# Kernel tuning notes

Measured on AMD Instinct MI355X. Metric: run time of the kernel, lower is better.

## Reference

```python
import jax, jax.numpy as jnp
import numpy as np

VOCAB = 50000   # vocab.count
EMBED = 256     # args.embed
B = 16          # batch
C = 64          # uniform context_len per example (stack() requires it)
S = 512         # src_seq == qry_seq == args.max_in_seq
UNK = 1         # vocab.w2i['<UNK>']


def setup_inputs() -> dict:
    key = jax.random.key(0)
    k1, k2, k3, k4 = jax.random.split(key, 4)
    sources = jax.random.randint(k1, (B * C, S), 0, VOCAB)
    # queries: contiguous nonzero prefix of length q_len in [S//2, S], zeros after
    ids = jax.random.randint(k2, (B, S), 1, VOCAB)
    qlens = jax.random.randint(k3, (B,), S // 2, S + 1)
    queries = jnp.where(jnp.arange(S)[None, :] < qlens[:, None], ids, 0)
    emb = jax.random.normal(k4, (VOCAB, EMBED), dtype=jnp.float32)
    return {"sources": sources, "queries": queries, "context_len": C, "emb": emb}


def reference(sources, queries, context_len, emb):
    vocab = emb.shape[0]
    # unk_tensor: clamp out-of-vocab ids to <UNK>
    src_ids = jnp.where(sources >= vocab, UNK, sources)
    q_ids = jnp.where(queries >= vocab, UNK, queries)
    b, s = queries.shape
    # [b, C, S, D] embedded sources; [b, S, D] embedded queries
    es = emb[src_ids].reshape(b, context_len, s, emb.shape[1])
    eq = emb[q_ids]
    # q_len slicing == masking since nonzero query prefix is contiguous
    qmask = (queries > 0).astype(emb.dtype)            # [b, S]
    # score[b,c] = sum_{j < q_len_b} <es[b,c,j], eq[b,j]>
    scores = jnp.einsum('bcsd,bsd->bc', es, eq * qmask[:, :, None])
    sims = jax.nn.softmax(scores, axis=1)              # per-example softmax over context
    top = jnp.argmax(scores, axis=1)                   # argmax of sim == argmax of scores
    src3 = sources.reshape(b, context_len, s)
    out_sources = jnp.take_along_axis(src3, top[:, None, None], axis=1).squeeze(1)
    return out_sources, sims
```

## Files before the change

### kernel.cpp

```cpp
#include <hip/hip_runtime.h>

#define VOCAB 50000
#define EMBED 256
#define NB    16
#define NC    64
#define NS    512
#define UNK   1

#define NPART 8
#define PDIV  ((VOCAB + NPART - 1) / NPART)
#define PJT   8
#define PJLEN 64
#define WLCAP 1024
#define NSLICE (NPART * PJT)
#define BF_TABLE_BYTES ((size_t)VOCAB * EMBED * 2)
#define PARTIAL_ELEMS  (NSLICE * NB * NC)

__device__ __forceinline__ unsigned short f2bf_rne(float f) {
    unsigned int u = __float_as_uint(f);
    u = (u + 0x7fffu + ((u >> 16) & 1u)) >> 16;
    return (unsigned short)u;
}

__global__ __launch_bounds__(256) void convert_kernel(
    const float* __restrict__ emb, unsigned int* __restrict__ bf)
{
    const size_t t = (size_t)blockIdx.x * 256 + threadIdx.x;
    const float4* __restrict__ e4 = (const float4*)emb;
    const float4 a = e4[t * 2];
    const float4 b = e4[t * 2 + 1];
    uint4 r;
    r.x = (unsigned int)f2bf_rne(a.x) | ((unsigned int)f2bf_rne(a.y) << 16);
    r.y = (unsigned int)f2bf_rne(a.z) | ((unsigned int)f2bf_rne(a.w) << 16);
    r.z = (unsigned int)f2bf_rne(b.x) | ((unsigned int)f2bf_rne(b.y) << 16);
    r.w = (unsigned int)f2bf_rne(b.z) | ((unsigned int)f2bf_rne(b.w) << 16);
    ((uint4*)bf)[t] = r;
}

__device__ __forceinline__ float dot_u(unsigned a, unsigned b) {
    const float a0 = __uint_as_float(a << 16);
    const float a1 = __uint_as_float(a & 0xffff0000u);
    const float b0 = __uint_as_float(b << 16);
    const float b1 = __uint_as_float(b & 0xffff0000u);
    return a0 * b0 + a1 * b1;
}

__global__ __launch_bounds__(256) void scores_part_kernel(
    const int* __restrict__ src, const int* __restrict__ q,
    const unsigned int* __restrict__ bf, float* __restrict__ partial)
{
    const int bid = blockIdx.x;
    const int p   = bid & (NPART - 1);
    const int jt  = (bid >> 3) & (PJT - 1);
    const int b   = bid >> 6;
    const int j0  = jt * PJLEN;

    const int tid  = threadIdx.x;
    const int wave = tid >> 6;
    const int lane = tid & 63;
    const int half = lane >> 5;
    const int hl   = lane & 31;

    const uint2* __restrict__ bfe  = (const uint2*)bf;
    const uint4* __restrict__ bft4 = (const uint4*)bf;

    __shared__ uint2 qt[PJLEN][64];
    __shared__ unsigned int wl[WLCAP];
    __shared__ float score_sh[NC];
    __shared__ int qid_sh[PJLEN];
    __shared__ int cnt;

    if (tid < PJLEN) {
        const int qv = q[(size_t)b * NS + j0 + tid];
        qid_sh[tid] = (qv == 0) ? -1 : ((qv >= VOCAB) ? UNK : qv);
    }
    if (tid < NC) score_sh[tid] = 0.f;
    if (tid == 0) cnt = 0;
    __syncthreads();

    for (int r = wave; r < PJLEN; r += 4) {
        const int qid = qid_sh[r];
        if (qid >= 0)
            qt[r][lane] = bfe[(size_t)qid * 64 + lane];
    }

    const int* __restrict__ srow = src + (size_t)b * NC * NS;
#pragma unroll
    for (int k = 0; k < 16; k++) {
        const int idx = k * 256 + tid;
        const int c   = idx >> 6;
        const int jj  = idx & 63;
        int sv = srow[(size_t)c * NS + j0 + jj];
        sv = (sv >= VOCAB) ? UNK : sv;
        if (qid_sh[jj] >= 0 && (sv / PDIV) == p) {
            const int pos = atomicAdd(&cnt, 1);
            if (pos < WLCAP)
                wl[pos] = ((unsigned)sv << 12) | (unsigned)(c << 6) | (unsigned)jj;
        }
    }
    __syncthreads();

    const int nE = (cnt < WLCAP) ? cnt : WLCAP;

    for (int e = wave * 2; e < nE; e += 16) {
        const int eA = e + half;
        const int eB = e + 8 + half;
        const bool vA = eA < nE;
        const bool vB = eB < nE;
        const unsigned wA = wl[vA ? eA : 0];
        const unsigned wB = wl[vB ? eB : 0];
        const int sidA = wA >> 12, cA = (wA >> 6) & 63, jA = wA & 63;
        const int sidB = wB >> 12, cB = (wB >> 6) & 63, jB = wB & 63;
        const uint4 gA = bft4[(size_t)sidA * 32 + hl];
        const uint4 gB = bft4[(size_t)sidB * 32 + hl];
        const uint4 qA = ((const uint4*)qt[jA])[hl];
        const uint4 qB = ((const uint4*)qt[jB])[hl];
        float dA = dot_u(gA.x, qA.x) + dot_u(gA.y, qA.y)
                 + dot_u(gA.z, qA.z) + dot_u(gA.w, qA.w);
        float dB = dot_u(gB.x, qB.x) + dot_u(gB.y, qB.y)
                 + dot_u(gB.z, qB.z) + dot_u(gB.w, qB.w);
#pragma unroll
        for (int off = 16; off > 0; off >>= 1) {
            dA += __shfl_down(dA, off, 32);
            dB += __shfl_down(dB, off, 32);
        }
        if (hl == 0) {
            if (vA) atomicAdd(&score_sh[cA], dA);
            if (vB) atomicAdd(&score_sh[cB], dB);
        }
    }
    __syncthreads();

    if (tid < NC)
        partial[(size_t)(p * PJT + jt) * (NB * NC) + b * NC + tid] = score_sh[tid];
}

__global__ __launch_bounds__(256) void scores_f32_kernel(
    const int* __restrict__ src, const int* __restrict__ q,
    const float* __restrict__ emb, float* __restrict__ partial)
{
    const int x  = blockIdx.x;
    const int jt = x & 7;
    const int ct = (x >> 3) & 7;
    const int b  = x >> 6;
    const int c0 = ct * 8;
    const int j0 = jt * 64;

    const int tid = threadIdx.x, wave = tid >> 6, lane = tid & 63;
    const float4* __restrict__ emb4 = (const float4*)emb;
    const int* __restrict__ qrow = q + (size_t)b * NS;
    const int* __restrict__ srow = src + ((size_t)b * NC + c0) * NS;

    float acc[8];
#pragma unroll
    for (int i = 0; i < 8; i++) acc[i] = 0.f;

    for (int j = j0 + wave; j < j0 + 64; j += 4) {
        const int qv = qrow[j];
        if (qv > 0) {
            const int qid = (qv >= VOCAB) ? UNK : qv;
            const float4 eq = emb4[(size_t)qid * (EMBED / 4) + lane];
            float4 a[8];
#pragma unroll
            for (int i = 0; i < 8; i++) {
                const int sv = srow[(size_t)i * NS + j];
                a[i] = emb4[(size_t)((sv >= VOCAB) ? UNK : sv) * (EMBED / 4) + lane];
            }
#pragma unroll
            for (int i = 0; i < 8; i++)
                acc[i] += a[i].x * eq.x + a[i].y * eq.y + a[i].z * eq.z + a[i].w * eq.w;
        }
    }
#pragma unroll
    for (int off = 32; off > 0; off >>= 1)
#pragma unroll
        for (int i = 0; i < 8; i++)
            acc[i] += __shfl_down(acc[i], off, 64);

    __shared__ float red[4][8];
    if (lane == 0)
#pragma unroll
        for (int i = 0; i < 8; i++) red[wave][i] = acc[i];
    __syncthreads();
    if (tid < 8)
        partial[(size_t)jt * (NB * NC) + b * NC + c0 + tid] =
            red[0][tid] + red[1][tid] + red[2][tid] + red[3][tid];
}

__global__ __launch_bounds__(256) void finalize_kernel(
    const float* __restrict__ partial, const int* __restrict__ src,
    float* __restrict__ out, int jtn)
{
    const int b = blockIdx.x, tid = threadIdx.x;
    __shared__ int top_sh;

    if (tid < 64) {
        float s = 0.f;
        for (int t = 0; t < jtn; t++)
            s += partial[(size_t)t * (NB * NC) + b * NC + tid];

        float m = s;
#pragma unroll
        for (int off = 32; off > 0; off >>= 1)
            m = fmaxf(m, __shfl_xor(m, off, 64));
        const float e = expf(s - m);
        float sum = e;
#pragma unroll
        for (int off = 32; off > 0; off >>= 1)
            sum += __shfl_xor(sum, off, 64);

        out[NB * NS + b * NC + tid] = e / sum;

        const unsigned long long ballot = __ballot(s == m);
        if (tid == 0) top_sh = __ffsll(ballot) - 1;
    }
    __syncthreads();

    const int top = top_sh;
    const int* __restrict__ srow = src + ((size_t)b * NC + top) * NS;
    for (int j = tid; j < NS; j += 256)
        out[b * NS + j] = (float)srow[j];
}

extern "C" void kernel_launch(void* const* d_in, const int* in_sizes, int n_in,
                              void* d_out, int out_size, void* d_ws, size_t ws_size,
                              hipStream_t stream) {
    const int*   src = (const int*)d_in[0];
    const int*   q   = (const int*)d_in[1];
    const float* emb = (const float*)d_in[3];
    float* out = (float*)d_out;

    if (ws_size >= BF_TABLE_BYTES + PARTIAL_ELEMS * sizeof(float)) {
        unsigned int* bf = (unsigned int*)d_ws;
        float* partial = (float*)((char*)d_ws + BF_TABLE_BYTES);
        convert_kernel<<<VOCAB * EMBED / 2048, 256, 0, stream>>>(emb, bf);
        scores_part_kernel<<<NB * PJT * NPART, 256, 0, stream>>>(src, q, bf, partial);
        finalize_kernel<<<NB, 256, 0, stream>>>(partial, src, out, NSLICE);
    } else {
        float* partial = (float*)d_ws;
        scores_f32_kernel<<<NB * 8 * 8, 256, 0, stream>>>(src, q, emb, partial);
        finalize_kernel<<<NB, 256, 0, stream>>>(partial, src, out, 8);
    }
}
```

Before: 149.3 us.

## Remap dot-product work to 4 lanes per entry with padded query tile and ballot compaction

The scores kernel now gives each worklist entry to 4 lanes, each reading 128 contiguous bytes of the gathered bf16 row, in place of a 32-lane half-wave per entry. This puts 16 entries in flight per wave and cuts shuffle-reduction depth. The query tile is stored with a padded row stride to reduce LDS bank conflicts on these wider reads, and is loaded with 16-byte vectors. Worklist appends use a wave ballot with one atomic per wave instead of one atomic per element, and the partition test becomes a range check instead of a division. The trade-off is more registers per lane, and each lane now issues sequential 16-byte gather loads rather than the old coalesced half-wave access.

```diff
diff --git a/kernel.cpp b/kernel.cpp
--- a/kernel.cpp
+++ b/kernel.cpp
@@ -12,6 +12,7 @@
 #define PJT   8
 #define PJLEN 64
 #define WLCAP 1024
+#define QSTRIDE 528
 #define NSLICE (NPART * PJT)
 #define BF_TABLE_BYTES ((size_t)VOCAB * EMBED * 2)
 #define PARTIAL_ELEMS  (NSLICE * NB * NC)
@@ -58,13 +59,11 @@
     const int tid  = threadIdx.x;
     const int wave = tid >> 6;
     const int lane = tid & 63;
-    const int half = lane >> 5;
-    const int hl   = lane & 31;
-
-    const uint2* __restrict__ bfe  = (const uint2*)bf;
+    const int sub  = lane & 3;
+
     const uint4* __restrict__ bft4 = (const uint4*)bf;
 
-    __shared__ uint2 qt[PJLEN][64];
+    __shared__ unsigned char qt_raw[PJLEN * QSTRIDE];
     __shared__ unsigned int wl[WLCAP];
     __shared__ float score_sh[NC];
     __shared__ int qid_sh[PJLEN];
@@ -78,12 +77,19 @@
     if (tid == 0) cnt = 0;
     __syncthreads();
 
-    for (int r = wave; r < PJLEN; r += 4) {
-        const int qid = qid_sh[r];
-        if (qid >= 0)
-            qt[r][lane] = bfe[(size_t)qid * 64 + lane];
-    }
-
+#pragma unroll
+    for (int i = 0; i < 8; i++) {
+        const int idx = i * 256 + tid;
+        const int row = idx >> 5;
+        const int col = idx & 31;
+        const int qid = qid_sh[row];
+        if (qid >= 0) {
+            const uint4 v = bft4[(size_t)qid * 32 + col];
+            *(uint4*)(qt_raw + row * QSTRIDE + col * 16) = v;
+        }
+    }
+
+    const int lo = p * PDIV;
     const int* __restrict__ srow = src + (size_t)b * NC * NS;
 #pragma unroll
     for (int k = 0; k < 16; k++) {
@@ -92,8 +98,13 @@
         const int jj  = idx & 63;
         int sv = srow[(size_t)c * NS + j0 + jj];
         sv = (sv >= VOCAB) ? UNK : sv;
-        if (qid_sh[jj] >= 0 && (sv / PDIV) == p) {
-            const int pos = atomicAdd(&cnt, 1);
+        const bool take = (qid_sh[jj] >= 0) && ((unsigned)(sv - lo) < (unsigned)PDIV);
+        const unsigned long long bal = __ballot(take);
+        int base = 0;
+        if (lane == 0 && bal != 0ull) base = atomicAdd(&cnt, __popcll(bal));
+        base = __shfl(base, 0, 64);
+        if (take) {
+            const int pos = base + __popcll(bal & ((1ull << lane) - 1ull));
             if (pos < WLCAP)
                 wl[pos] = ((unsigned)sv << 12) | (unsigned)(c << 6) | (unsigned)jj;
         }
@@ -102,32 +113,26 @@
 
     const int nE = (cnt < WLCAP) ? cnt : WLCAP;
 
-    for (int e = wave * 2; e < nE; e += 16) {
-        const int eA = e + half;
-        const int eB = e + 8 + half;
-        const bool vA = eA < nE;
-        const bool vB = eB < nE;
-        const unsigned wA = wl[vA ? eA : 0];
-        const unsigned wB = wl[vB ? eB : 0];
-        const int sidA = wA >> 12, cA = (wA >> 6) & 63, jA = wA & 63;
-        const int sidB = wB >> 12, cB = (wB >> 6) & 63, jB = wB & 63;
-        const uint4 gA = bft4[(size_t)sidA * 32 + hl];
-        const uint4 gB = bft4[(size_t)sidB * 32 + hl];
-        const uint4 qA = ((const uint4*)qt[jA])[hl];
-        const uint4 qB = ((const uint4*)qt[jB])[hl];
-        float dA = dot_u(gA.x, qA.x) + dot_u(gA.y, qA.y)
-                 + dot_u(gA.z, qA.z) + dot_u(gA.w, qA.w);
-        float dB = dot_u(gB.x, qB.x) + dot_u(gB.y, qB.y)
-                 + dot_u(gB.z, qB.z) + dot_u(gB.w, qB.w);
-#pragma unroll
-        for (int off = 16; off > 0; off >>= 1) {
-            dA += __shfl_down(dA, off, 32);
-            dB += __shfl_down(dB, off, 32);
-        }
-        if (hl == 0) {
-            if (vA) atomicAdd(&score_sh[cA], dA);
-            if (vB) atomicAdd(&score_sh[cB], dB);
-        }
+    for (int e0 = wave * 16; e0 < nE; e0 += 64) {
+        const int e = e0 + (lane >> 2);
+        const bool valid = e < nE;
+        const unsigned w = wl[valid ? e : 0];
+        const int sid = (int)(w >> 12);
+        const int c   = (int)((w >> 6) & 63u);
+        const int j   = (int)(w & 63u);
+        const uint4* __restrict__ grow = bft4 + (size_t)sid * 32 + sub * 8;
+        const unsigned char* qbase = qt_raw + j * QSTRIDE + sub * 128;
+        float acc = 0.f;
+#pragma unroll
+        for (int k = 0; k < 8; k++) {
+            const uint4 g  = grow[k];
+            const uint4 qv = *(const uint4*)(qbase + k * 16);
+            acc += dot_u(g.x, qv.x) + dot_u(g.y, qv.y)
+                 + dot_u(g.z, qv.z) + dot_u(g.w, qv.w);
+        }
+        acc += __shfl_down(acc, 2, 4);
+        acc += __shfl_down(acc, 1, 4);
+        if (valid && sub == 0) atomicAdd(&score_sh[c], acc);
     }
     __syncthreads();
 
```

Result: slower. 154.7 us (+3.6%).
